# Kernel tuning notes

Measured on AMD Instinct MI355X. Metric: run time of the kernel, lower is better.

Reference implementation:

```python
import jax, jax.numpy as jnp
import numpy as np

N_NODES = 50000
N_EDGES = 600000
IN_CH, HID1, HID2, OUT_CH = 128, 256, 128, 2


def setup_inputs() -> dict:
    key = jax.random.key(0)
    ks = jax.random.split(key, 8)
    x = jax.random.normal(ks[0], (N_NODES, IN_CH), dtype=jnp.float32)
    edge_index = jax.random.randint(ks[1], (2, N_EDGES), 0, N_NODES, dtype=jnp.int64)
    # Glorot-style init for GCN linear weights
    def glorot(k, fan_in, fan_out):
        s = jnp.sqrt(6.0 / (fan_in + fan_out)).astype(jnp.float32)
        return jax.random.uniform(k, (fan_in, fan_out), jnp.float32, -s, s)
    return {
        "x": x,
        "W1": glorot(ks[2], IN_CH, HID1), "b1": jnp.zeros((HID1,), jnp.float32),
        "W2": glorot(ks[3], HID1, HID2), "b2": jnp.zeros((HID2,), jnp.float32),
        "W3": glorot(ks[4], HID2, OUT_CH), "b3": jnp.zeros((OUT_CH,), jnp.float32),
        "edge_index": edge_index,
    }


def _gcn_graph(edge_index, n_nodes):
    # Add self-loops (GCNConv default) and compute symmetric normalization
    loop = jnp.arange(n_nodes, dtype=edge_index.dtype)
    src = jnp.concatenate([edge_index[0], loop])
    dst = jnp.concatenate([edge_index[1], loop])
    ones = jnp.ones(src.shape[0], dtype=jnp.float32)
    deg = jax.ops.segment_sum(ones, dst, num_segments=n_nodes)
    dinv = jnp.where(deg > 0, jax.lax.rsqrt(deg), 0.0)
    norm = dinv[src] * dinv[dst]  # [E + N]
    return src, dst, norm


def _gcn_layer(h, W, b, src, dst, norm, n_nodes):
    h = h @ W                                   # [N, d_out]
    msg = h[src] * norm[:, None]                # gather + scale  [E+N, d_out]
    agg = jax.ops.segment_sum(msg, dst, num_segments=n_nodes)
    return agg + b


def reference(x, W1, b1, W2, b2, W3, b3, edge_index):
    n = x.shape[0]
    src, dst, norm = _gcn_graph(edge_index, n)
    h = jax.nn.relu(_gcn_layer(x, W1, b1, src, dst, norm, n))
    # dropout p=0.5 is identity in eval mode (training=False)
    h = jax.nn.relu(_gcn_layer(h, W2, b2, src, dst, norm, n))
    h = _gcn_layer(h, W3, b3, src, dst, norm, n)
    return jax.nn.log_softmax(h, axis=1)
```

## Files before the change

### kernel.cpp

```cpp
#include <hip/hip_runtime.h>
#include <hip/hip_bf16.h>
#include <math.h>

#define N_NODES 50000
#define N_EDGES 600000
#define E_TOT   (N_EDGES + N_NODES)
#define M_PAD   50048
#define NODE_STRIDE 64
#define CSR_CAP (N_NODES * NODE_STRIDE + 2048)

typedef __attribute__((ext_vector_type(8))) short bf16x8;
typedef __attribute__((ext_vector_type(4))) float f32x4;
typedef __attribute__((ext_vector_type(8))) unsigned short u16x8;


__device__ __forceinline__ unsigned short f2bf(float f) {
    unsigned int u = __float_as_uint(f);
    unsigned int r = (u + 0x7fffu + ((u >> 16) & 1u)) >> 16;
    return (unsigned short)r;
}

__device__ __forceinline__ void acc_row(float* acc, uint4 v) {
    acc[0] += __uint_as_float(v.x << 16);
    acc[1] += __uint_as_float(v.x & 0xffff0000u);
    acc[2] += __uint_as_float(v.y << 16);
    acc[3] += __uint_as_float(v.y & 0xffff0000u);
    acc[4] += __uint_as_float(v.z << 16);
    acc[5] += __uint_as_float(v.z & 0xffff0000u);
    acc[6] += __uint_as_float(v.w << 16);
    acc[7] += __uint_as_float(v.w & 0xffff0000u);
}

#define GLD_LDS16(g, l) __builtin_amdgcn_global_load_lds( \
    (__attribute__((address_space(1))) void*)(void*)(g), \
    (__attribute__((address_space(3))) void*)(l), 16, 0, 0)


__global__ void prep_kernel(const int* __restrict__ ei, int* __restrict__ cnt,
                            int* __restrict__ pos,
                            const float* __restrict__ W1, const float* __restrict__ W2,
                            unsigned short* __restrict__ W1t, unsigned short* __restrict__ W2t,
                            unsigned short* __restrict__ csr, unsigned short* __restrict__ xs) {
    const int NB_E = (N_EDGES + 255) / 256;
    const int NB_F = (CSR_CAP / 8 + 255) / 256;
    int b = blockIdx.x;
    if (b < NB_E) {
        int e = b * 256 + threadIdx.x;
        if (e < N_EDGES) pos[e] = atomicAdd(&cnt[ei[N_EDGES + e]], 1);
    } else if (b < NB_E + 128) {
        int i = (b - NB_E) * 256 + threadIdx.x;
        int k = i >> 8, n = i & 255;
        W1t[(size_t)n * 128 + k] = f2bf(W1[i]);
    } else if (b < NB_E + 256) {
        int i = (b - NB_E - 128) * 256 + threadIdx.x;
        int k = i >> 7, n = i & 127;
        W2t[(size_t)n * 256 + k] = f2bf(W2[i]);
    } else if (b < NB_E + 256 + NB_F) {
        int i = (b - NB_E - 256) * 256 + threadIdx.x;
        if (i >= CSR_CAP / 8) return;
        const unsigned int dd = 0xC350C350u;
        *(uint4*)(csr + (size_t)i * 8) = make_uint4(dd, dd, dd, dd);
    } else {
        if (threadIdx.x < 16)
            *(uint4*)(xs + (size_t)N_NODES * 128 + threadIdx.x * 8) = make_uint4(0, 0, 0, 0);
    }
}


__global__ void fill_kernel(const int* __restrict__ ei, const int* __restrict__ cnt,
                            const int* __restrict__ pos, unsigned short* __restrict__ csr,
                            const float* __restrict__ x, unsigned short* __restrict__ xs,
                            float* __restrict__ dinv) {
    const int NB_A = (E_TOT + 255) / 256;
    const int NB_C = (N_NODES * 32 + 255) / 256;
    int b = blockIdx.x;
    if (b < NB_A) {
        int e = b * 256 + threadIdx.x;
        if (e >= E_TOT) return;
        if (e < N_EDGES) {
            int s = ei[e], d = ei[N_EDGES + e];
            csr[(d << 6) + pos[e]] = (unsigned short)s;
        } else {
            int i = e - N_EDGES;
            csr[(i << 6) + cnt[i]] = (unsigned short)i;
        }
    } else if (b < NB_A + NB_C) {
        int i = (b - NB_A) * 256 + threadIdx.x;
        if (i >= N_NODES * 32) return;
        float d = rsqrtf((float)(cnt[i >> 5] + 1));
        float4 v = *(const float4*)(x + (size_t)i * 4);
        ushort4 o;
        o.x = f2bf(v.x * d); o.y = f2bf(v.y * d); o.z = f2bf(v.z * d); o.w = f2bf(v.w * d);
        *(ushort4*)(xs + (size_t)i * 4) = o;
    } else {
        int i = (b - NB_A - NB_C) * 256 + threadIdx.x;
        if (i < N_NODES) dinv[i] = rsqrtf((float)(cnt[i] + 1));
    }
}


template<bool LAYER2>
__global__ __launch_bounds__(256) void agg_kernel(
    const unsigned short* __restrict__ Hs, const float* __restrict__ dinv,
    const int* __restrict__ cnt, const unsigned short* __restrict__ csr,
    const float* __restrict__ bias, const float* __restrict__ W3,
    unsigned short* __restrict__ outb, float2* __restrict__ Ts) {
    int wave = threadIdx.x >> 6;
    int lane = threadIdx.x & 63;
    int n = blockIdx.x * 4 + wave;
    if (LAYER2 && blockIdx.x == 0 && threadIdx.x == 0) Ts[N_NODES] = make_float2(0.f, 0.f);
    if (n >= N_NODES) return;
    int quarter = lane >> 4;
    int q = lane & 15;
    float acc[8] = {};
    int p0 = n << 6;
    int pend = p0 + ((cnt[n] + 16) & ~15);
    int p = p0 + quarter * 4;
    ushort4 s4 = *(const ushort4*)(csr + p);
    while (p < pend) {
        int pn = p + 16;
        ushort4 n4 = *(const ushort4*)(csr + pn);
        uint4 v0 = *(const uint4*)(Hs + (size_t)s4.x * 128 + q * 8);
        uint4 v1 = *(const uint4*)(Hs + (size_t)s4.y * 128 + q * 8);
        uint4 v2 = *(const uint4*)(Hs + (size_t)s4.z * 128 + q * 8);
        uint4 v3 = *(const uint4*)(Hs + (size_t)s4.w * 128 + q * 8);
        acc_row(acc, v0);
        acc_row(acc, v1);
        acc_row(acc, v2);
        acc_row(acc, v3);
        p = pn; s4 = n4;
    }
    #pragma unroll
    for (int i = 0; i < 8; ++i) {
        acc[i] += __shfl_xor(acc[i], 16);
        acc[i] += __shfl_xor(acc[i], 32);
    }
    float dn = dinv[n];
    if (!LAYER2) {
        if (quarter == 0) {
            u16x8 ov;
            #pragma unroll
            for (int i = 0; i < 8; ++i) ov[i] = f2bf(acc[i] * dn);
            *(u16x8*)(outb + (size_t)n * 128 + q * 8) = ov;
        }
    } else {
        float t0 = 0.f, t1 = 0.f;
        #pragma unroll
        for (int i = 0; i < 8; ++i) {
            int c = q * 8 + i;
            float h = fmaxf(acc[i] * dn + bias[c], 0.f);
            float2 w = ((const float2*)W3)[c];
            t0 += h * w.x; t1 += h * w.y;
        }
        #pragma unroll
        for (int off = 1; off < 16; off <<= 1) {
            t0 += __shfl_xor(t0, off);
            t1 += __shfl_xor(t1, off);
        }
        if (lane == 0) Ts[n] = make_float2(t0 * dn, t1 * dn);
    }
}


__global__ __launch_bounds__(256) void gemm12_kernel(
    const unsigned short* __restrict__ A,
    const unsigned short* __restrict__ W1t,
    const unsigned short* __restrict__ W2t,
    const float* __restrict__ b1,
    const float* __restrict__ rowscale,
    unsigned short* __restrict__ C,
    int M) {
    __shared__ __align__(16) unsigned short h1buf[128 * 256];
    __shared__ __align__(16) unsigned short As[128 * 32];
    __shared__ __align__(16) unsigned short Bs[64 * 32];
    int tid = threadIdx.x;
    int wave = tid >> 6, lane = tid & 63;
    int m0 = blockIdx.x * 128;
    int mm = lane & 15, kg = lane >> 4;
    int row0 = kg * 4;

    int am[2];
    #pragma unroll
    for (int i = 0; i < 2; ++i) {
        int m = wave * 32 + i * 16 + mm;
        am[i] = (m * 4 + (kg ^ ((m >> 1) & 3))) * 8;
    }
    int bn[4];
    #pragma unroll
    for (int j = 0; j < 4; ++j) {
        int n = j * 16 + mm;
        bn[j] = (n * 4 + (kg ^ ((n >> 1) & 3))) * 8;
    }
    int h1rd[2];
    #pragma unroll
    for (int i = 0; i < 2; ++i) {
        int m = wave * 32 + i * 16 + mm;
        h1rd[i] = m * 32 * 8;
    }

    #pragma unroll 1
    for (int nt = 0; nt < 4; ++nt) {
        int n0 = nt * 64;
        f32x4 acc[2][4];
        #pragma unroll
        for (int i = 0; i < 2; ++i)
            #pragma unroll
            for (int j = 0; j < 4; ++j)
                acc[i][j] = (f32x4){0.f, 0.f, 0.f, 0.f};
        #pragma unroll 1
        for (int k0 = 0; k0 < 128; k0 += 32) {
            #pragma unroll
            for (int iss = 0; iss < 2; ++iss) {
                int ci = iss * 256 + tid;
                int r = ci >> 2, c8s = ci & 3;
                int c8 = c8s ^ ((r >> 1) & 3);
                const unsigned short* g = A + (size_t)(m0 + r) * 128 + k0 + c8 * 8;
                unsigned short* l = As + (size_t)(iss * 256 + (tid & 192)) * 8;
                GLD_LDS16(g, l);
            }
            {
                int r = tid >> 2, c8s = tid & 3;
                int c8 = c8s ^ ((r >> 1) & 3);
                const unsigned short* g = W1t + (size_t)(n0 + r) * 128 + k0 + c8 * 8;
                unsigned short* l = Bs + (size_t)(tid & 192) * 8;
                GLD_LDS16(g, l);
            }
            __syncthreads();
            bf16x8 af[2], bfr[4];
            #pragma unroll
            for (int i = 0; i < 2; ++i) af[i] = *(const bf16x8*)(As + am[i]);
            #pragma unroll
            for (int j = 0; j < 4; ++j) bfr[j] = *(const bf16x8*)(Bs + bn[j]);
            #pragma unroll
            for (int i = 0; i < 2; ++i)
                #pragma unroll
                for (int j = 0; j < 4; ++j)
                    acc[i][j] = __builtin_amdgcn_mfma_f32_16x16x32_bf16(af[i], bfr[j], acc[i][j], 0, 0, 0);
            __syncthreads();
        }
        float bj[4];
        #pragma unroll
        for (int j = 0; j < 4; ++j) bj[j] = b1[n0 + j * 16 + mm];
        #pragma unroll
        for (int i = 0; i < 2; ++i) {
            #pragma unroll
            for (int r = 0; r < 4; ++r) {
                int ml = wave * 32 + i * 16 + row0 + r;
                int rb = ml * 32 * 8, rx = ml & 15;
                #pragma unroll
                for (int j = 0; j < 4; ++j) {
                    int c = n0 + j * 16 + mm;
                    int c8 = c >> 3;
                    float v = fmaxf(acc[i][j][r] + bj[j], 0.f);
                    h1buf[rb + ((c8 ^ rx) * 8) + (c & 7)] = f2bf(v);
                }
            }
        }
    }
    __syncthreads();

    #pragma unroll 1
    for (int nh = 0; nh < 2; ++nh) {
        int n0 = nh * 64;
        f32x4 acc[2][4];
        #pragma unroll
        for (int i = 0; i < 2; ++i)
            #pragma unroll
            for (int j = 0; j < 4; ++j)
                acc[i][j] = (f32x4){0.f, 0.f, 0.f, 0.f};
        #pragma unroll 1
        for (int k0 = 0; k0 < 256; k0 += 32) {
            {
                int r = tid >> 2, c8s = tid & 3;
                int c8 = c8s ^ ((r >> 1) & 3);
                const unsigned short* g = W2t + (size_t)(n0 + r) * 256 + k0 + c8 * 8;
                unsigned short* l = Bs + (size_t)(tid & 192) * 8;
                GLD_LDS16(g, l);
            }
            __syncthreads();
            bf16x8 af[2], bfr[4];
            #pragma unroll
            for (int i = 0; i < 2; ++i) {
                int m = wave * 32 + i * 16 + mm;
                int c8 = (k0 >> 3) + kg;
                af[i] = *(const bf16x8*)(h1buf + h1rd[i] + ((c8 ^ (m & 15)) * 8));
            }
            #pragma unroll
            for (int j = 0; j < 4; ++j) bfr[j] = *(const bf16x8*)(Bs + bn[j]);
            #pragma unroll
            for (int i = 0; i < 2; ++i)
                #pragma unroll
                for (int j = 0; j < 4; ++j)
                    acc[i][j] = __builtin_amdgcn_mfma_f32_16x16x32_bf16(af[i], bfr[j], acc[i][j], 0, 0, 0);
            __syncthreads();
        }
        #pragma unroll
        for (int i = 0; i < 2; ++i) {
            #pragma unroll
            for (int r = 0; r < 4; ++r) {
                int gm = m0 + wave * 32 + i * 16 + row0 + r;
                float sc = (gm < M) ? rowscale[gm] : 0.f;
                #pragma unroll
                for (int j = 0; j < 4; ++j) {
                    int gn = n0 + j * 16 + mm;
                    C[(size_t)gm * 128 + gn] = f2bf(acc[i][j][r] * sc);
                }
            }
        }
    }
}


__global__ void lsm_kernel(const float2* __restrict__ Ts, const float* __restrict__ dinv,
                           const int* __restrict__ cnt, const unsigned short* __restrict__ csr,
                           const float* __restrict__ b3, float* __restrict__ out) {
    int n = blockIdx.x * 256 + threadIdx.x;
    if (n >= N_NODES) return;
    float a0 = 0.f, a1 = 0.f;
    int p0 = n << 6;
    int pend = p0 + ((cnt[n] + 16) & ~15);
    ushort4 s4 = *(const ushort4*)(csr + p0);
    for (int p = p0; p < pend; p += 4) {
        ushort4 n4 = *(const ushort4*)(csr + p + 4);
        float2 u0 = Ts[s4.x], u1 = Ts[s4.y], u2 = Ts[s4.z], u3 = Ts[s4.w];
        a0 += (u0.x + u1.x) + (u2.x + u3.x);
        a1 += (u0.y + u1.y) + (u2.y + u3.y);
        s4 = n4;
    }
    float dn = dinv[n];
    float v0 = a0 * dn + b3[0];
    float v1 = a1 * dn + b3[1];
    float m = fmaxf(v0, v1);
    float lse = m + logf(expf(v0 - m) + expf(v1 - m));
    out[n * 2 + 0] = v0 - lse;
    out[n * 2 + 1] = v1 - lse;
}


extern "C" void kernel_launch(void* const* d_in, const int* in_sizes, int n_in,
                              void* d_out, int out_size, void* d_ws, size_t ws_size,
                              hipStream_t stream) {
    const float* x  = (const float*)d_in[0];
    const float* W1 = (const float*)d_in[1];
    const float* b1 = (const float*)d_in[2];
    const float* W2 = (const float*)d_in[3];
    const float* b2 = (const float*)d_in[4];
    const float* W3 = (const float*)d_in[5];
    const float* b3 = (const float*)d_in[6];
    const int*   ei = (const int*)d_in[7];
    float* out = (float*)d_out;

    char* ws = (char*)d_ws;
    size_t off = 0;
    auto alloc = [&](size_t bytes) -> char* {
        char* p = ws + off;
        off = (off + bytes + 255) & ~(size_t)255;
        return p;
    };
    int*   cnt  = (int*)alloc(N_NODES * 4);
    int*   pos  = (int*)alloc(N_EDGES * 4);
    float* dinv = (float*)alloc(N_NODES * 4);
    unsigned short* csr = (unsigned short*)alloc((size_t)CSR_CAP * 2);
    unsigned short* xs     = (unsigned short*)alloc((size_t)(N_NODES + 1) * 128 * 2);
    unsigned short* W1t    = (unsigned short*)alloc((size_t)256 * 128 * 2);
    unsigned short* W2t    = (unsigned short*)alloc((size_t)128 * 256 * 2);
    unsigned short* aggx_b = (unsigned short*)alloc((size_t)M_PAD * 128 * 2);
    unsigned short* t2b    = (unsigned short*)alloc((size_t)M_PAD * 128 * 2);
    float2* Ts = (float2*)alloc((size_t)(N_NODES + 1) * 8);

    hipMemsetAsync(cnt, 0, N_NODES * 4, stream);

    const int NB_E = (N_EDGES + 255) / 256;
    const int NB_F = (CSR_CAP / 8 + 255) / 256;
    prep_kernel<<<NB_E + 256 + NB_F + 1, 256, 0, stream>>>(
        ei, cnt, pos, W1, W2, W1t, W2t, csr, xs);

    const int NB_A = (E_TOT + 255) / 256;
    const int NB_C = (N_NODES * 32 + 255) / 256;
    const int NB_D = (N_NODES + 255) / 256;
    fill_kernel<<<NB_A + NB_C + NB_D, 256, 0, stream>>>(ei, cnt, pos, csr, x, xs, dinv);

    agg_kernel<false><<<(N_NODES + 3) / 4, 256, 0, stream>>>(
        xs, dinv, cnt, csr, nullptr, nullptr, aggx_b, nullptr);
    gemm12_kernel<<<M_PAD / 128, 256, 0, stream>>>(
        aggx_b, W1t, W2t, b1, dinv, t2b, N_NODES);
    agg_kernel<true><<<(N_NODES + 3) / 4, 256, 0, stream>>>(
        t2b, dinv, cnt, csr, b2, W3, nullptr, Ts);

    lsm_kernel<<<(N_NODES + 255) / 256, 256, 0, stream>>>(Ts, dinv, cnt, csr, b3, out);
}
```

Measured before the change: 205.6 us.

## Build CSR in one atomic pass and handle self-loops separately

Edges are now written straight into the padded CSR slot returned by the atomic counter, which removes the pos array and the second scatter pass over edges. Self-loops are no longer stored in the CSR; each aggregation adds the node's own row explicitly, so the padded edge count shrinks by one. CSR padding now uses a memset to 0xFF that points at a zeroed dummy row 65535, which needs larger row allocations. The atomic scatter order becomes nondeterministic, which can change fp summation order slightly.

```diff
diff --git a/kernel.cpp b/kernel.cpp
--- a/kernel.cpp
+++ b/kernel.cpp
@@ -4,10 +4,11 @@
 
 #define N_NODES 50000
 #define N_EDGES 600000
-#define E_TOT   (N_EDGES + N_NODES)
 #define M_PAD   50048
 #define NODE_STRIDE 64
 #define CSR_CAP (N_NODES * NODE_STRIDE + 2048)
+#define DUMMY_ROW 65535
+#define ROWS_ALLOC 65536
 
 typedef __attribute__((ext_vector_type(8))) short bf16x8;
 typedef __attribute__((ext_vector_type(4))) float f32x4;
@@ -37,64 +38,53 @@
 
 
 __global__ void prep_kernel(const int* __restrict__ ei, int* __restrict__ cnt,
-                            int* __restrict__ pos,
+                            unsigned short* __restrict__ csr,
                             const float* __restrict__ W1, const float* __restrict__ W2,
-                            unsigned short* __restrict__ W1t, unsigned short* __restrict__ W2t,
-                            unsigned short* __restrict__ csr, unsigned short* __restrict__ xs) {
+                            unsigned short* __restrict__ W1t, unsigned short* __restrict__ W2t) {
     const int NB_E = (N_EDGES + 255) / 256;
-    const int NB_F = (CSR_CAP / 8 + 255) / 256;
     int b = blockIdx.x;
     if (b < NB_E) {
         int e = b * 256 + threadIdx.x;
-        if (e < N_EDGES) pos[e] = atomicAdd(&cnt[ei[N_EDGES + e]], 1);
+        if (e < N_EDGES) {
+            int s = ei[e], d = ei[N_EDGES + e];
+            int slot = atomicAdd(&cnt[d], 1);
+            csr[(d << 6) + slot] = (unsigned short)s;
+        }
     } else if (b < NB_E + 128) {
         int i = (b - NB_E) * 256 + threadIdx.x;
         int k = i >> 8, n = i & 255;
         W1t[(size_t)n * 128 + k] = f2bf(W1[i]);
-    } else if (b < NB_E + 256) {
+    } else {
         int i = (b - NB_E - 128) * 256 + threadIdx.x;
         int k = i >> 7, n = i & 127;
         W2t[(size_t)n * 256 + k] = f2bf(W2[i]);
-    } else if (b < NB_E + 256 + NB_F) {
-        int i = (b - NB_E - 256) * 256 + threadIdx.x;
-        if (i >= CSR_CAP / 8) return;
-        const unsigned int dd = 0xC350C350u;
-        *(uint4*)(csr + (size_t)i * 8) = make_uint4(dd, dd, dd, dd);
-    } else {
-        if (threadIdx.x < 16)
-            *(uint4*)(xs + (size_t)N_NODES * 128 + threadIdx.x * 8) = make_uint4(0, 0, 0, 0);
-    }
-}
-
-
-__global__ void fill_kernel(const int* __restrict__ ei, const int* __restrict__ cnt,
-                            const int* __restrict__ pos, unsigned short* __restrict__ csr,
+    }
+}
+
+
+__global__ void fill_kernel(const int* __restrict__ cnt,
                             const float* __restrict__ x, unsigned short* __restrict__ xs,
-                            float* __restrict__ dinv) {
-    const int NB_A = (E_TOT + 255) / 256;
+                            unsigned short* __restrict__ t2b, float* __restrict__ dinv) {
     const int NB_C = (N_NODES * 32 + 255) / 256;
+    const int NB_D = (N_NODES + 255) / 256;
     int b = blockIdx.x;
-    if (b < NB_A) {
-        int e = b * 256 + threadIdx.x;
-        if (e >= E_TOT) return;
-        if (e < N_EDGES) {
-            int s = ei[e], d = ei[N_EDGES + e];
-            csr[(d << 6) + pos[e]] = (unsigned short)s;
-        } else {
-            int i = e - N_EDGES;
-            csr[(i << 6) + cnt[i]] = (unsigned short)i;
-        }
-    } else if (b < NB_A + NB_C) {
-        int i = (b - NB_A) * 256 + threadIdx.x;
+    if (b < NB_C) {
+        int i = b * 256 + threadIdx.x;
         if (i >= N_NODES * 32) return;
         float d = rsqrtf((float)(cnt[i >> 5] + 1));
         float4 v = *(const float4*)(x + (size_t)i * 4);
         ushort4 o;
         o.x = f2bf(v.x * d); o.y = f2bf(v.y * d); o.z = f2bf(v.z * d); o.w = f2bf(v.w * d);
         *(ushort4*)(xs + (size_t)i * 4) = o;
+    } else if (b < NB_C + NB_D) {
+        int i = (b - NB_C) * 256 + threadIdx.x;
+        if (i < N_NODES) dinv[i] = rsqrtf((float)(cnt[i] + 1));
     } else {
-        int i = (b - NB_A - NB_C) * 256 + threadIdx.x;
-        if (i < N_NODES) dinv[i] = rsqrtf((float)(cnt[i] + 1));
+        int t = threadIdx.x;
+        if (t < 16)
+            *(uint4*)(xs + (size_t)DUMMY_ROW * 128 + t * 8) = make_uint4(0, 0, 0, 0);
+        else if (t < 32)
+            *(uint4*)(t2b + (size_t)DUMMY_ROW * 128 + (t - 16) * 8) = make_uint4(0, 0, 0, 0);
     }
 }
 
@@ -108,15 +98,18 @@
     int wave = threadIdx.x >> 6;
     int lane = threadIdx.x & 63;
     int n = blockIdx.x * 4 + wave;
-    if (LAYER2 && blockIdx.x == 0 && threadIdx.x == 0) Ts[N_NODES] = make_float2(0.f, 0.f);
+    if (LAYER2 && blockIdx.x == 0 && threadIdx.x == 0)
+        Ts[DUMMY_ROW] = make_float2(0.f, 0.f);
     if (n >= N_NODES) return;
     int quarter = lane >> 4;
     int q = lane & 15;
     float acc[8] = {};
     int p0 = n << 6;
-    int pend = p0 + ((cnt[n] + 16) & ~15);
+    int pend = p0 + ((cnt[n] + 15) & ~15);
     int p = p0 + quarter * 4;
     ushort4 s4 = *(const ushort4*)(csr + p);
+    if (quarter == 0)
+        acc_row(acc, *(const uint4*)(Hs + (size_t)n * 128 + q * 8));
     while (p < pend) {
         int pn = p + 16;
         ushort4 n4 = *(const ushort4*)(csr + pn);
@@ -316,9 +309,10 @@
                            const float* __restrict__ b3, float* __restrict__ out) {
     int n = blockIdx.x * 256 + threadIdx.x;
     if (n >= N_NODES) return;
-    float a0 = 0.f, a1 = 0.f;
+    float2 self = Ts[n];
+    float a0 = self.x, a1 = self.y;
     int p0 = n << 6;
-    int pend = p0 + ((cnt[n] + 16) & ~15);
+    int pend = p0 + ((cnt[n] + 15) & ~15);
     ushort4 s4 = *(const ushort4*)(csr + p0);
     for (int p = p0; p < pend; p += 4) {
         ushort4 n4 = *(const ushort4*)(csr + p + 4);
@@ -358,27 +352,24 @@
         return p;
     };
     int*   cnt  = (int*)alloc(N_NODES * 4);
-    int*   pos  = (int*)alloc(N_EDGES * 4);
     float* dinv = (float*)alloc(N_NODES * 4);
     unsigned short* csr = (unsigned short*)alloc((size_t)CSR_CAP * 2);
-    unsigned short* xs     = (unsigned short*)alloc((size_t)(N_NODES + 1) * 128 * 2);
-    unsigned short* W1t    = (unsigned short*)alloc((size_t)256 * 128 * 2);
-    unsigned short* W2t    = (unsigned short*)alloc((size_t)128 * 256 * 2);
+    unsigned short* xs  = (unsigned short*)alloc((size_t)ROWS_ALLOC * 128 * 2);
+    unsigned short* W1t = (unsigned short*)alloc((size_t)256 * 128 * 2);
+    unsigned short* W2t = (unsigned short*)alloc((size_t)128 * 256 * 2);
     unsigned short* aggx_b = (unsigned short*)alloc((size_t)M_PAD * 128 * 2);
-    unsigned short* t2b    = (unsigned short*)alloc((size_t)M_PAD * 128 * 2);
-    float2* Ts = (float2*)alloc((size_t)(N_NODES + 1) * 8);
+    unsigned short* t2b    = (unsigned short*)alloc((size_t)ROWS_ALLOC * 128 * 2);
+    float2* Ts = (float2*)alloc((size_t)ROWS_ALLOC * 8);
 
     hipMemsetAsync(cnt, 0, N_NODES * 4, stream);
+    hipMemsetAsync(csr, 0xFF, (size_t)CSR_CAP * 2, stream);
 
     const int NB_E = (N_EDGES + 255) / 256;
-    const int NB_F = (CSR_CAP / 8 + 255) / 256;
-    prep_kernel<<<NB_E + 256 + NB_F + 1, 256, 0, stream>>>(
-        ei, cnt, pos, W1, W2, W1t, W2t, csr, xs);
-
-    const int NB_A = (E_TOT + 255) / 256;
+    prep_kernel<<<NB_E + 256, 256, 0, stream>>>(ei, cnt, csr, W1, W2, W1t, W2t);
+
     const int NB_C = (N_NODES * 32 + 255) / 256;
     const int NB_D = (N_NODES + 255) / 256;
-    fill_kernel<<<NB_A + NB_C + NB_D, 256, 0, stream>>>(ei, cnt, pos, csr, x, xs, dinv);
+    fill_kernel<<<NB_C + NB_D + 1, 256, 0, stream>>>(cnt, x, xs, t2b, dinv);
 
     agg_kernel<false><<<(N_NODES + 3) / 4, 256, 0, stream>>>(
         xs, dinv, cnt, csr, nullptr, nullptr, aggx_b, nullptr);
```

After: 210.8 us. 1.03x slower.
